# Kernel tuning notes

Hardware: AMD Instinct MI355X
Metric: run time of the kernel (lower is better)

The kernel has to match this reference:

```python
import jax, jax.numpy as jnp
import numpy as np

K = 1  # top-k from init_kwargs


def setup_inputs() -> dict:
    key = jax.random.key(0)
    k0, k1, k2, k3, k4, k5 = jax.random.split(key, 6)
    B, L, Ed, NE = 8192, 1024, 1024, 8
    D = L + Ed  # input_dim = latent_dim + embed_dim
    s = 1.0 / np.sqrt(D)  # torch nn.Linear default init bound
    x = jax.random.normal(k0, (B, L), dtype=jnp.float32)
    y = jax.random.normal(k1, (B, Ed), dtype=jnp.float32)
    We = jax.random.uniform(k2, (NE, D, D), dtype=jnp.float32, minval=-s, maxval=s)  # expert weights [E, out, in]
    be = jax.random.uniform(k3, (NE, D), dtype=jnp.float32, minval=-s, maxval=s)
    gW = jax.random.uniform(k4, (NE, D), dtype=jnp.float32, minval=-s, maxval=s)  # gate weight [E, in]
    gb = jax.random.uniform(k5, (NE,), dtype=jnp.float32, minval=-s, maxval=s)
    return {"x": x, "y": y, "We": We, "be": be, "gW": gW, "gb": gb}


def reference(x, y, We, be, gW, gb):
    # inp: [B, D]
    inp = jnp.concatenate([x, y], axis=1)
    # gate logits: [B, E] (eval mode: no noise)
    gate_logits = inp @ gW.T + gb
    topk_val, topk_idx = jax.lax.top_k(gate_logits, K)  # [B, K]
    topk_gates = jax.nn.softmax(topk_val, axis=1)       # [B, K]
    # dense compute-all-experts (faithful to original): [B, E, D]
    all_out = jnp.einsum('bd,eod->beo', inp, We) + be[None, :, :]
    # gather top-k experts per token: [B, K, D]
    gathered = jnp.take_along_axis(all_out, topk_idx[:, :, None], axis=1)
    fused = jnp.sum(gathered * topk_gates[:, :, None], axis=1)  # [B, D]
    return fused
```

## Files before the change

kernel.cpp:

```cpp
#include <hip/hip_runtime.h>
#include <stdint.h>

#define B_TOK 8192
#define DIM   2048
#define NE    8
#define BM 128
#define BN 128
#define BK 64
#define CVT_BLOCKS 8192

#define BK2 32
#define NT2 (DIM / BK2)

typedef __bf16 bf16x8 __attribute__((ext_vector_type(8)));
typedef float  f32x4  __attribute__((ext_vector_type(4)));

__device__ __forceinline__ unsigned short f2b(float f) {
  unsigned u = __builtin_bit_cast(unsigned, f);
  u += 0x7fffu + ((u >> 16) & 1u);
  return (unsigned short)(u >> 16);
}
__device__ __forceinline__ uint2 pack4(float4 v) {
  uint2 r;
  r.x = (unsigned)f2b(v.x) | ((unsigned)f2b(v.y) << 16);
  r.y = (unsigned)f2b(v.z) | ((unsigned)f2b(v.w) << 16);
  return r;
}
__device__ __forceinline__ void gload16(const void* g, void* l) {
  __builtin_amdgcn_global_load_lds(
      (const __attribute__((address_space(1))) void*)g,
      (__attribute__((address_space(3))) void*)l, 16, 0, 0);
}

template <bool WINP>
__global__ __launch_bounds__(256) void gate_kernel(
    const float* __restrict__ x,
    const float* __restrict__ y,
    const float* __restrict__ gW,
    const float* __restrict__ gb,
    int* __restrict__ eid,
    unsigned short* __restrict__ inpB) {
  const int tid = threadIdx.x;
  const int ln = tid & 63;
  const int token = blockIdx.x * 4 + (tid >> 6);

  double acc[NE];
#pragma unroll
  for (int e = 0; e < NE; ++e) acc[e] = 0.0;

  const float* bases[2] = {x, y};
#pragma unroll
  for (int p = 0; p < 2; ++p) {
    const float* rowp = bases[p] + (size_t)token * 1024;
#pragma unroll
    for (int it = 0; it < 4; ++it) {
      const int d = it * 256 + ln * 4;
      float4 v = *(const float4*)(rowp + d);
      if (WINP)
        *(uint2*)(inpB + (size_t)token * DIM + p * 1024 + d) = pack4(v);
#pragma unroll
      for (int e = 0; e < NE; ++e) {
        float4 g = *(const float4*)(gW + e * DIM + p * 1024 + d);
        acc[e] += (double)v.x * (double)g.x + (double)v.y * (double)g.y +
                  (double)v.z * (double)g.z + (double)v.w * (double)g.w;
      }
    }
  }
#pragma unroll
  for (int e = 0; e < NE; ++e) {
#pragma unroll
    for (int off = 32; off >= 1; off >>= 1) acc[e] += __shfl_xor(acc[e], off, 64);
  }
  if (ln == 0) {
    int best = 0;
    double bv = acc[0] + (double)gb[0];
#pragma unroll
    for (int e = 1; e < NE; ++e) {
      double v = acc[e] + (double)gb[e];
      if (v > bv) { bv = v; best = e; }
    }
    eid[token] = best;
  }
}

template <bool CVT>
__global__ __launch_bounds__(256) void bucket_cvt(
    const int* __restrict__ eid,
    int* __restrict__ counts,
    int* __restrict__ perm,
    const float* __restrict__ We,
    unsigned short* __restrict__ WeB) {
  if (CVT && blockIdx.x >= NE) {
    const int cb = blockIdx.x - NE;
    const size_t base = (size_t)cb * 1024;
#pragma unroll
    for (int j = 0; j < 4; ++j) {
      size_t i4 = base + (size_t)(j * 256 + threadIdx.x);
      float4 v = *(const float4*)(We + i4 * 4);
      *(uint2*)(WeB + i4 * 4) = pack4(v);
    }
    return;
  }

  const int e = blockIdx.x;
  const int tid = threadIdx.x, ln = tid & 63, wv = tid >> 6;
  __shared__ int wsum[4];
  __shared__ int basev;
  if (tid == 0) basev = 0;
  __syncthreads();
  for (int t0 = 0; t0 < B_TOK; t0 += 256) {
    int t = t0 + tid;
    bool m = (eid[t] == e);
    unsigned long long mk = __ballot(m);
    int pre = __popcll(mk & ((1ull << ln) - 1ull));
    if (ln == 0) wsum[wv] = __popcll(mk);
    __syncthreads();
    int off = basev;
    for (int w = 0; w < wv; ++w) off += wsum[w];
    if (m) perm[e * B_TOK + off + pre] = t;
    __syncthreads();
    if (tid == 0) basev += wsum[0] + wsum[1] + wsum[2] + wsum[3];
    __syncthreads();
  }
  if (tid == 0) counts[e] = basev;
}

__global__ __launch_bounds__(256, 2) void moe_gemm2(
    const float* __restrict__ be,
    const unsigned short* __restrict__ inpB,
    const unsigned short* __restrict__ WeB,
    const int* __restrict__ counts,
    const int* __restrict__ perm,
    float* __restrict__ out) {
  __shared__ __align__(16) unsigned short AB[32768];
  __shared__ int tokLds[BM];

  const int e = blockIdx.z;
  const int cnt = counts[e];
  const int m0 = blockIdx.y * BM;
  if (m0 >= cnt) return;
  const int n0 = blockIdx.x * BN;

  const int tid = threadIdx.x;
  const int ln = tid & 63;
  const int wv = tid >> 6;
  const int wm = wv & 1, wn = wv >> 1;

  if (tid < BM) {
    int r = m0 + tid;
    tokLds[tid] = perm[e * B_TOK + (r < cnt ? r : cnt - 1)];
  }
  __syncthreads();

  const int srow0 = (wv * 2 + 0) * 16 + (ln >> 2);
  const int srow1 = (wv * 2 + 1) * 16 + (ln >> 2);
  const int g = (ln & 3) ^ ((ln >> 2) & 3);
  const unsigned short* wbbase = WeB + (size_t)e * DIM * DIM;
  const unsigned short* aSrc0 = inpB + (size_t)tokLds[srow0] * DIM + g * 8;
  const unsigned short* aSrc1 = inpB + (size_t)tokLds[srow1] * DIM + g * 8;
  const unsigned short* bSrc0 = wbbase + (size_t)(n0 + srow0) * DIM + g * 8;
  const unsigned short* bSrc1 = wbbase + (size_t)(n0 + srow1) * DIM + g * 8;
  const int dstA0 = (wv * 2 + 0) * 512;
  const int dstA1 = (wv * 2 + 1) * 512;

  const int slotR = (ln >> 4) ^ (ln & 3);
  const int aOff = (wm * 64 + (ln & 15)) * 32 + slotR * 8;
  const int bOff = (wn * 64 + (ln & 15)) * 32 + slotR * 8;

  f32x4 acc[4][4];
#pragma unroll
  for (int i = 0; i < 4; ++i)
#pragma unroll
    for (int j = 0; j < 4; ++j) acc[i][j] = (f32x4){0.f, 0.f, 0.f, 0.f};

  auto STAGE = [&](int kt) {
    const int b = (kt & 3) * 4096;
    const int ko = kt * BK2;
    gload16(aSrc0 + ko, &AB[b + dstA0]);
    gload16(aSrc1 + ko, &AB[b + dstA1]);
    gload16(bSrc0 + ko, &AB[16384 + b + dstA0]);
    gload16(bSrc1 + ko, &AB[16384 + b + dstA1]);
  };
  auto COMPUTE = [&](int kt) {
    const int b = (kt & 3) * 4096;
    bf16x8 av[4], bv[4];
#pragma unroll
    for (int i = 0; i < 4; ++i)
      av[i] = *(const bf16x8*)&AB[b + aOff + i * 512];
#pragma unroll
    for (int j = 0; j < 4; ++j)
      bv[j] = *(const bf16x8*)&AB[16384 + b + bOff + j * 512];
    __builtin_amdgcn_s_setprio(1);
#pragma unroll
    for (int i = 0; i < 4; ++i)
#pragma unroll
      for (int j = 0; j < 4; ++j)
        acc[i][j] = __builtin_amdgcn_mfma_f32_16x16x32_bf16(av[i], bv[j], acc[i][j], 0, 0, 0);
    __builtin_amdgcn_s_setprio(0);
  };

  STAGE(0); STAGE(1); STAGE(2);
  asm volatile("s_waitcnt vmcnt(8)" ::: "memory");
  __builtin_amdgcn_s_barrier();

  for (int t = 0; t < NT2; ++t) {
    if (t + 3 < NT2) STAGE(t + 3);
    COMPUTE(t);
    if (t < NT2 - 3) {
      asm volatile("s_waitcnt vmcnt(8)" ::: "memory");
    } else if (t == NT2 - 3) {
      asm volatile("s_waitcnt vmcnt(4)" ::: "memory");
    } else if (t == NT2 - 2) {
      asm volatile("s_waitcnt vmcnt(0)" ::: "memory");
    }
    if (t < NT2 - 1) __builtin_amdgcn_s_barrier();
  }

  float bias[4]; int col[4];
#pragma unroll
  for (int j = 0; j < 4; ++j) {
    col[j] = n0 + wn * 64 + j * 16 + (ln & 15);
    bias[j] = be[e * DIM + col[j]];
  }
#pragma unroll
  for (int i = 0; i < 4; ++i) {
    int rbase = wm * 64 + i * 16 + ((ln >> 4) << 2);
#pragma unroll
    for (int r = 0; r < 4; ++r) {
      int rl = rbase + r;
      if (m0 + rl < cnt) {
        size_t t = (size_t)tokLds[rl];
#pragma unroll
        for (int j = 0; j < 4; ++j)
          out[t * DIM + col[j]] = acc[i][j][r] + bias[j];
      }
    }
  }
}

__global__ __launch_bounds__(256) void moe_gemm_f32(
    const float* __restrict__ x,
    const float* __restrict__ y,
    const float* __restrict__ We,
    const float* __restrict__ be,
    const int* __restrict__ counts,
    const int* __restrict__ perm,
    float* __restrict__ out) {
  __shared__ unsigned short As[BM * BK];
  __shared__ unsigned short Bs[BN * BK];
  __shared__ int tokLds[BM];

  const int e = blockIdx.z;
  const int cnt = counts[e];
  const int m0 = blockIdx.y * BM;
  if (m0 >= cnt) return;
  const int n0 = blockIdx.x * BN;

  const int tid = threadIdx.x;
  const int ln = tid & 63;
  const int wv = tid >> 6;
  const int wm = wv & 1, wn = wv >> 1;

  if (tid < BM) {
    int r = m0 + tid;
    tokLds[tid] = perm[e * B_TOK + (r < cnt ? r : cnt - 1)];
  }
  __syncthreads();

  const float* wfbase = We + (size_t)e * DIM * DIM;

  f32x4 acc[4][4];
#pragma unroll
  for (int i = 0; i < 4; ++i)
#pragma unroll
    for (int j = 0; j < 4; ++j) acc[i][j] = (f32x4){0.f, 0.f, 0.f, 0.f};

  for (int k0 = 0; k0 < DIM; k0 += BK) {
    __syncthreads();
    const float* ab = (k0 < 1024) ? x : y;
    const int kk = k0 & 1023;
#pragma unroll
    for (int i = 0; i < 8; ++i) {
      int li = i * 256 + tid;
      int row = li >> 4, k4 = li & 15;
      int chunk = k4 >> 1, half = k4 & 1;
      int slot = (chunk ^ (row & 7)) * 2 + half;
      int tok = tokLds[row];
      float4 va = *(const float4*)(ab + (size_t)tok * 1024 + kk + k4 * 4);
      *(uint2*)&As[row * BK + slot * 4] = pack4(va);
      float4 vb = *(const float4*)(wfbase + (size_t)(n0 + row) * DIM + k0 + k4 * 4);
      *(uint2*)&Bs[row * BK + slot * 4] = pack4(vb);
    }
    __syncthreads();

#pragma unroll
    for (int ks = 0; ks < 2; ++ks) {
      bf16x8 av[4], bv[4];
#pragma unroll
      for (int i = 0; i < 4; ++i) {
        int rA = wm * 64 + i * 16 + (ln & 15);
        int c = ks * 4 + (ln >> 4);
        av[i] = *(const bf16x8*)&As[rA * BK + (c ^ (rA & 7)) * 8];
      }
#pragma unroll
      for (int j = 0; j < 4; ++j) {
        int rB = wn * 64 + j * 16 + (ln & 15);
        int c = ks * 4 + (ln >> 4);
        bv[j] = *(const bf16x8*)&Bs[rB * BK + (c ^ (rB & 7)) * 8];
      }
#pragma unroll
      for (int i = 0; i < 4; ++i)
#pragma unroll
        for (int j = 0; j < 4; ++j)
          acc[i][j] = __builtin_amdgcn_mfma_f32_16x16x32_bf16(av[i], bv[j], acc[i][j], 0, 0, 0);
    }
  }

  float bias[4]; int col[4];
#pragma unroll
  for (int j = 0; j < 4; ++j) {
    col[j] = n0 + wn * 64 + j * 16 + (ln & 15);
    bias[j] = be[e * DIM + col[j]];
  }
#pragma unroll
  for (int i = 0; i < 4; ++i) {
    int rbase = wm * 64 + i * 16 + ((ln >> 4) << 2);
#pragma unroll
    for (int r = 0; r < 4; ++r) {
      int rl = rbase + r;
      if (m0 + rl < cnt) {
        size_t t = (size_t)tokLds[rl];
#pragma unroll
        for (int j = 0; j < 4; ++j)
          out[t * DIM + col[j]] = acc[i][j][r] + bias[j];
      }
    }
  }
}

extern "C" void kernel_launch(void* const* d_in, const int* in_sizes, int n_in,
                              void* d_out, int out_size, void* d_ws, size_t ws_size,
                              hipStream_t stream) {
  const float* x  = (const float*)d_in[0];
  const float* y  = (const float*)d_in[1];
  const float* We = (const float*)d_in[2];
  const float* be = (const float*)d_in[3];
  const float* gW = (const float*)d_in[4];
  const float* gb = (const float*)d_in[5];
  float* out = (float*)d_out;

  char* ws = (char*)d_ws;
  int* counts = (int*)ws;
  int* eid    = (int*)(ws + 256);
  int* perm   = (int*)(ws + 33024);
  unsigned short* inpB = (unsigned short*)(ws + 295168);
  unsigned short* WeB  = (unsigned short*)(ws + 33849600);
  const size_t needed = 33849600ull + 67108864ull;

  if (ws_size >= needed) {
    gate_kernel<true><<<dim3(B_TOK / 4), 256, 0, stream>>>(x, y, gW, gb, eid, inpB);
    bucket_cvt<true><<<dim3(NE + CVT_BLOCKS), 256, 0, stream>>>(eid, counts, perm, We, WeB);
    moe_gemm2<<<dim3(DIM / BN, B_TOK / BM, NE), 256, 0, stream>>>(
        be, inpB, WeB, counts, perm, out);
  } else {
    gate_kernel<false><<<dim3(B_TOK / 4), 256, 0, stream>>>(x, y, gW, gb, eid, nullptr);
    bucket_cvt<false><<<dim3(NE), 256, 0, stream>>>(eid, counts, perm, nullptr, nullptr);
    moe_gemm_f32<<<dim3(DIM / BN, B_TOK / BM, NE), 256, 0, stream>>>(
        x, y, We, be, counts, perm, out);
  }
}
```

Baseline: 440.7 us.

## Use 256x256 tiles with 8 waves in the grouped expert GEMM; fuse weight conversion into gate

The grouped expert GEMM now uses 256x256 output tiles, 512 threads, BK=64 double buffering and four sub-phases per k-step, with the next stage's loads issued between phases. An XOR-swizzled LDS layout holds 64-wide k rows. The fp32-to-bf16 weight conversion moves from the bucketing kernel into the gate kernel, so the bucketing kernel launches only 8 blocks. The larger tiles raise arithmetic intensity per LDS byte but use 128KB LDS and many more accumulators, and they add padding waste for experts whose token count is not a multiple of 256.

```diff
diff --git a/kernel.cpp b/kernel.cpp
--- a/kernel.cpp
+++ b/kernel.cpp
@@ -8,9 +8,8 @@
 #define BN 128
 #define BK 64
 #define CVT_BLOCKS 8192
-
-#define BK2 32
-#define NT2 (DIM / BK2)
+#define GATE_BLOCKS 2048
+#define NT3 32
 
 typedef __bf16 bf16x8 __attribute__((ext_vector_type(8)));
 typedef float  f32x4  __attribute__((ext_vector_type(4)));
@@ -32,17 +31,32 @@
       (__attribute__((address_space(3))) void*)l, 16, 0, 0);
 }
 
-template <bool WINP>
-__global__ __launch_bounds__(256) void gate_kernel(
+template <bool FULL>
+__global__ __launch_bounds__(256) void gate_cvt(
     const float* __restrict__ x,
     const float* __restrict__ y,
     const float* __restrict__ gW,
     const float* __restrict__ gb,
+    const float* __restrict__ We,
     int* __restrict__ eid,
-    unsigned short* __restrict__ inpB) {
+    unsigned short* __restrict__ inpB,
+    unsigned short* __restrict__ WeB) {
+  const int bid = blockIdx.x;
+  if (FULL && bid >= GATE_BLOCKS) {
+    const int cb = bid - GATE_BLOCKS;
+    const size_t base = (size_t)cb * 1024;
+#pragma unroll
+    for (int j = 0; j < 4; ++j) {
+      size_t i4 = base + (size_t)(j * 256 + threadIdx.x);
+      float4 v = *(const float4*)(We + i4 * 4);
+      *(uint2*)(WeB + i4 * 4) = pack4(v);
+    }
+    return;
+  }
+
   const int tid = threadIdx.x;
   const int ln = tid & 63;
-  const int token = blockIdx.x * 4 + (tid >> 6);
+  const int token = bid * 4 + (tid >> 6);
 
   double acc[NE];
 #pragma unroll
@@ -56,7 +70,7 @@
     for (int it = 0; it < 4; ++it) {
       const int d = it * 256 + ln * 4;
       float4 v = *(const float4*)(rowp + d);
-      if (WINP)
+      if (FULL)
         *(uint2*)(inpB + (size_t)token * DIM + p * 1024 + d) = pack4(v);
 #pragma unroll
       for (int e = 0; e < NE; ++e) {
@@ -83,25 +97,9 @@
   }
 }
 
-template <bool CVT>
-__global__ __launch_bounds__(256) void bucket_cvt(
-    const int* __restrict__ eid,
-    int* __restrict__ counts,
-    int* __restrict__ perm,
-    const float* __restrict__ We,
-    unsigned short* __restrict__ WeB) {
-  if (CVT && blockIdx.x >= NE) {
-    const int cb = blockIdx.x - NE;
-    const size_t base = (size_t)cb * 1024;
-#pragma unroll
-    for (int j = 0; j < 4; ++j) {
-      size_t i4 = base + (size_t)(j * 256 + threadIdx.x);
-      float4 v = *(const float4*)(We + i4 * 4);
-      *(uint2*)(WeB + i4 * 4) = pack4(v);
-    }
-    return;
-  }
-
+__global__ __launch_bounds__(256) void bucket8(const int* __restrict__ eid,
+                                               int* __restrict__ counts,
+                                               int* __restrict__ perm) {
   const int e = blockIdx.x;
   const int tid = threadIdx.x, ln = tid & 63, wv = tid >> 6;
   __shared__ int wsum[4];
@@ -125,114 +123,131 @@
   if (tid == 0) counts[e] = basev;
 }
 
-__global__ __launch_bounds__(256, 2) void moe_gemm2(
+__global__ __launch_bounds__(512, 2) void moe_gemm3(
     const float* __restrict__ be,
     const unsigned short* __restrict__ inpB,
     const unsigned short* __restrict__ WeB,
     const int* __restrict__ counts,
     const int* __restrict__ perm,
     float* __restrict__ out) {
-  __shared__ __align__(16) unsigned short AB[32768];
-  __shared__ int tokLds[BM];
+  __shared__ __align__(16) unsigned short AB[65536];
+  __shared__ int tokLds[256];
 
   const int e = blockIdx.z;
   const int cnt = counts[e];
-  const int m0 = blockIdx.y * BM;
+  const int m0 = blockIdx.y * 256;
   if (m0 >= cnt) return;
-  const int n0 = blockIdx.x * BN;
+  const int n0 = blockIdx.x * 256;
 
   const int tid = threadIdx.x;
   const int ln = tid & 63;
   const int wv = tid >> 6;
-  const int wm = wv & 1, wn = wv >> 1;
-
-  if (tid < BM) {
+  const int wm = wv & 1;
+  const int wn = wv >> 1;
+
+  if (tid < 256) {
     int r = m0 + tid;
     tokLds[tid] = perm[e * B_TOK + (r < cnt ? r : cnt - 1)];
   }
   __syncthreads();
 
-  const int srow0 = (wv * 2 + 0) * 16 + (ln >> 2);
-  const int srow1 = (wv * 2 + 1) * 16 + (ln >> 2);
-  const int g = (ln & 3) ^ ((ln >> 2) & 3);
+  const int g = (ln & 7) ^ (ln >> 3);
   const unsigned short* wbbase = WeB + (size_t)e * DIM * DIM;
-  const unsigned short* aSrc0 = inpB + (size_t)tokLds[srow0] * DIM + g * 8;
-  const unsigned short* aSrc1 = inpB + (size_t)tokLds[srow1] * DIM + g * 8;
-  const unsigned short* bSrc0 = wbbase + (size_t)(n0 + srow0) * DIM + g * 8;
-  const unsigned short* bSrc1 = wbbase + (size_t)(n0 + srow1) * DIM + g * 8;
-  const int dstA0 = (wv * 2 + 0) * 512;
-  const int dstA1 = (wv * 2 + 1) * 512;
-
-  const int slotR = (ln >> 4) ^ (ln & 3);
-  const int aOff = (wm * 64 + (ln & 15)) * 32 + slotR * 8;
-  const int bOff = (wn * 64 + (ln & 15)) * 32 + slotR * 8;
-
-  f32x4 acc[4][4];
-#pragma unroll
-  for (int i = 0; i < 4; ++i)
-#pragma unroll
-    for (int j = 0; j < 4; ++j) acc[i][j] = (f32x4){0.f, 0.f, 0.f, 0.f};
-
-  auto STAGE = [&](int kt) {
-    const int b = (kt & 3) * 4096;
-    const int ko = kt * BK2;
-    gload16(aSrc0 + ko, &AB[b + dstA0]);
-    gload16(aSrc1 + ko, &AB[b + dstA1]);
-    gload16(bSrc0 + ko, &AB[16384 + b + dstA0]);
-    gload16(bSrc1 + ko, &AB[16384 + b + dstA1]);
+  const unsigned short* aS[2][2];
+  const unsigned short* bS[2][2];
+#pragma unroll
+  for (int h = 0; h < 2; ++h)
+#pragma unroll
+    for (int i = 0; i < 2; ++i) {
+      int row = h * 128 + (wv * 2 + i) * 8 + (ln >> 3);
+      aS[h][i] = inpB + (size_t)tokLds[row] * DIM + g * 8;
+      bS[h][i] = wbbase + (size_t)(n0 + row) * DIM + g * 8;
+    }
+
+  f32x4 acc[8][4];
+#pragma unroll
+  for (int a = 0; a < 8; ++a)
+#pragma unroll
+    for (int b = 0; b < 4; ++b) acc[a][b] = (f32x4){0.f, 0.f, 0.f, 0.f};
+
+  auto STG = [&](int kt, int h) {
+    const int d = (kt & 1) * 16384;
+    const int ko = kt * 64;
+    gload16(aS[h][0] + ko, &AB[d + h * 8192 + (wv * 2 + 0) * 512]);
+    gload16(aS[h][1] + ko, &AB[d + h * 8192 + (wv * 2 + 1) * 512]);
+    gload16(bS[h][0] + ko, &AB[32768 + d + h * 8192 + (wv * 2 + 0) * 512]);
+    gload16(bS[h][1] + ko, &AB[32768 + d + h * 8192 + (wv * 2 + 1) * 512]);
   };
-  auto COMPUTE = [&](int kt) {
-    const int b = (kt & 3) * 4096;
-    bf16x8 av[4], bv[4];
-#pragma unroll
-    for (int i = 0; i < 4; ++i)
-      av[i] = *(const bf16x8*)&AB[b + aOff + i * 512];
-#pragma unroll
-    for (int j = 0; j < 4; ++j)
-      bv[j] = *(const bf16x8*)&AB[16384 + b + bOff + j * 512];
+
+  auto PHASE = [&](int kt, int mh, int nh) {
+    const int d = (kt & 1) * 16384;
+    bf16x8 av[4][2], bv[2][2];
+#pragma unroll
+    for (int f = 0; f < 4; ++f)
+#pragma unroll
+      for (int ks = 0; ks < 2; ++ks) {
+        int r = wm * 128 + mh * 64 + f * 16 + (ln & 15);
+        int c = ks * 4 + (ln >> 4);
+        av[f][ks] = *(const bf16x8*)&AB[d + r * 64 + ((c ^ (ln & 7))) * 8];
+      }
+#pragma unroll
+    for (int j = 0; j < 2; ++j)
+#pragma unroll
+      for (int ks = 0; ks < 2; ++ks) {
+        int r = wn * 64 + nh * 32 + j * 16 + (ln & 15);
+        int c = ks * 4 + (ln >> 4);
+        bv[j][ks] = *(const bf16x8*)&AB[32768 + d + r * 64 + ((c ^ (ln & 7))) * 8];
+      }
     __builtin_amdgcn_s_setprio(1);
 #pragma unroll
-    for (int i = 0; i < 4; ++i)
-#pragma unroll
-      for (int j = 0; j < 4; ++j)
-        acc[i][j] = __builtin_amdgcn_mfma_f32_16x16x32_bf16(av[i], bv[j], acc[i][j], 0, 0, 0);
+    for (int f = 0; f < 4; ++f)
+#pragma unroll
+      for (int j = 0; j < 2; ++j)
+#pragma unroll
+        for (int ks = 0; ks < 2; ++ks)
+          acc[mh * 4 + f][nh * 2 + j] = __builtin_amdgcn_mfma_f32_16x16x32_bf16(
+              av[f][ks], bv[j][ks], acc[mh * 4 + f][nh * 2 + j], 0, 0, 0);
     __builtin_amdgcn_s_setprio(0);
   };
 
-  STAGE(0); STAGE(1); STAGE(2);
-  asm volatile("s_waitcnt vmcnt(8)" ::: "memory");
-  __builtin_amdgcn_s_barrier();
-
-  for (int t = 0; t < NT2; ++t) {
-    if (t + 3 < NT2) STAGE(t + 3);
-    COMPUTE(t);
-    if (t < NT2 - 3) {
-      asm volatile("s_waitcnt vmcnt(8)" ::: "memory");
-    } else if (t == NT2 - 3) {
+  STG(0, 0); STG(0, 1);
+
+  for (int kt = 0; kt < NT3; ++kt) {
+    if (kt + 1 < NT3) {
+      STG(kt + 1, 0);
       asm volatile("s_waitcnt vmcnt(4)" ::: "memory");
-    } else if (t == NT2 - 2) {
+    } else {
       asm volatile("s_waitcnt vmcnt(0)" ::: "memory");
     }
-    if (t < NT2 - 1) __builtin_amdgcn_s_barrier();
+    __builtin_amdgcn_s_barrier();
+    PHASE(kt, 0, 0);
+    __builtin_amdgcn_s_barrier();
+    if (kt + 1 < NT3) STG(kt + 1, 1);
+    PHASE(kt, 0, 1);
+    __builtin_amdgcn_s_barrier();
+    PHASE(kt, 1, 1);
+    __builtin_amdgcn_s_barrier();
+    PHASE(kt, 1, 0);
+    __builtin_amdgcn_s_barrier();
   }
 
   float bias[4]; int col[4];
 #pragma unroll
-  for (int j = 0; j < 4; ++j) {
-    col[j] = n0 + wn * 64 + j * 16 + (ln & 15);
-    bias[j] = be[e * DIM + col[j]];
-  }
-#pragma unroll
-  for (int i = 0; i < 4; ++i) {
-    int rbase = wm * 64 + i * 16 + ((ln >> 4) << 2);
+  for (int b = 0; b < 4; ++b) {
+    col[b] = n0 + wn * 64 + b * 16 + (ln & 15);
+    bias[b] = be[e * DIM + col[b]];
+  }
+#pragma unroll
+  for (int a = 0; a < 8; ++a) {
+    int rbase = wm * 128 + a * 16 + ((ln >> 4) << 2);
 #pragma unroll
     for (int r = 0; r < 4; ++r) {
       int rl = rbase + r;
       if (m0 + rl < cnt) {
         size_t t = (size_t)tokLds[rl];
 #pragma unroll
-        for (int j = 0; j < 4; ++j)
-          out[t * DIM + col[j]] = acc[i][j][r] + bias[j];
+        for (int b = 0; b < 4; ++b)
+          out[t * DIM + col[b]] = acc[a][b][r] + bias[b];
       }
     }
   }
@@ -358,13 +373,15 @@
   const size_t needed = 33849600ull + 67108864ull;
 
   if (ws_size >= needed) {
-    gate_kernel<true><<<dim3(B_TOK / 4), 256, 0, stream>>>(x, y, gW, gb, eid, inpB);
-    bucket_cvt<true><<<dim3(NE + CVT_BLOCKS), 256, 0, stream>>>(eid, counts, perm, We, WeB);
-    moe_gemm2<<<dim3(DIM / BN, B_TOK / BM, NE), 256, 0, stream>>>(
+    gate_cvt<true><<<dim3(GATE_BLOCKS + CVT_BLOCKS), 256, 0, stream>>>(
+        x, y, gW, gb, We, eid, inpB, WeB);
+    bucket8<<<dim3(NE), 256, 0, stream>>>(eid, counts, perm);
+    moe_gemm3<<<dim3(DIM / 256, B_TOK / 256, NE), 512, 0, stream>>>(
         be, inpB, WeB, counts, perm, out);
   } else {
-    gate_kernel<false><<<dim3(B_TOK / 4), 256, 0, stream>>>(x, y, gW, gb, eid, nullptr);
-    bucket_cvt<false><<<dim3(NE), 256, 0, stream>>>(eid, counts, perm, nullptr, nullptr);
+    gate_cvt<false><<<dim3(GATE_BLOCKS), 256, 0, stream>>>(
+        x, y, gW, gb, nullptr, eid, nullptr, nullptr);
+    bucket8<<<dim3(NE), 256, 0, stream>>>(eid, counts, perm);
     moe_gemm_f32<<<dim3(DIM / BN, B_TOK / BM, NE), 256, 0, stream>>>(
         x, y, We, be, counts, perm, out);
   }
```

Result: slower. 482.3 us (+9.4%).
